# Optimization experiments

Hardware: AMD Instinct MI355X
Metric: run time of the kernel (lower is better)

The kernel has to match this reference:

```python
import jax, jax.numpy as jnp
import numpy as np
from jax import lax

B, C, L = 8, 512, 4096
G, K = 4, 3
PAD = 1
EPS = 1e-5


def setup_inputs() -> dict:
    key = jax.random.key(0)
    ks = jax.random.split(key, 8)
    inp = {
        "input_feat": jax.random.normal(ks[0], (B, C, L), dtype=jnp.float32),
        "x": jax.random.normal(ks[1], (B, C, L), dtype=jnp.float32),
        # depthwise Conv1d(channels, channels, k=3, pad=1, groups=channels): weight (C,1,K)
        "conv_w": jax.random.normal(ks[2], (C, 1, K), dtype=jnp.float32) * (1.0 / np.sqrt(K)),
        "conv_b": jax.random.normal(ks[3], (C,), dtype=jnp.float32) * 0.02,
        # BatchNorm1d affine params (module maps 'LN' -> BatchNorm1d)
        "bn_gamma": jnp.ones((C,), dtype=jnp.float32),
        "bn_beta": jnp.zeros((C,), dtype=jnp.float32),
        # offset/weight generators: Linear(C -> G*K). Source inits to zero (degenerate);
        # use small random values so the deformable path is exercised.
        "off_w": jax.random.normal(ks[4], (G * K, C), dtype=jnp.float32) * 0.02,
        "off_b": jax.random.normal(ks[5], (G * K,), dtype=jnp.float32) * 0.02,
        "wgt_w": jax.random.normal(ks[6], (G * K, C), dtype=jnp.float32) * 0.02,
        "wgt_b": jax.random.normal(ks[7], (G * K,), dtype=jnp.float32) * 0.02,
    }
    return inp


def _forward(x, conv_w, conv_b, bn_gamma, bn_beta, off_w, off_b, wgt_w, wgt_b):
    Bx, Cx, Lx = x.shape
    gs = Cx // G  # group size along channel axis

    # --- spectral_conv: depthwise conv1d + BatchNorm (batch stats) + exact GELU ---
    y = lax.conv_general_dilated(
        x, conv_w, window_strides=(1,), padding=[(PAD, PAD)],
        dimension_numbers=("NCH", "OIH", "NCH"), feature_group_count=Cx,
    ) + conv_b[None, :, None]
    mean = jnp.mean(y, axis=(0, 2), keepdims=True)
    var = jnp.var(y, axis=(0, 2), keepdims=True)
    y = (y - mean) * lax.rsqrt(var + EPS) * bn_gamma[None, :, None] + bn_beta[None, :, None]
    y = jax.nn.gelu(y, approximate=False)  # torch nn.GELU default is exact erf

    feat = y.transpose(0, 2, 1)  # (B, L, C)
    offsets = (feat @ off_w.T + off_b).reshape(Bx, Lx, G, K)
    weights = jax.nn.softmax((feat @ wgt_w.T + wgt_b).reshape(Bx, Lx, G, K), axis=-1)

    # --- deformable spectral gather + bilinear interp + softmax blend ---
    xg = x.transpose(0, 2, 1).reshape(Bx, Lx, G, gs)  # (B, L, G, gs)
    base = jnp.arange(gs, dtype=x.dtype)
    # sample positions: (B, L, G, K, gs)
    idx = jnp.clip(base[None, None, None, None, :] + offsets[..., None], 0.0, gs - 1)
    fl = jnp.floor(idx)
    frac = idx - fl
    fli = jnp.clip(fl, 0, gs - 1).astype(jnp.int32)
    cei = jnp.clip(jnp.ceil(idx), 0, gs - 1).astype(jnp.int32)

    xe = jnp.broadcast_to(xg[:, :, :, None, :], idx.shape)  # (B, L, G, K, gs)
    x_floor = jnp.take_along_axis(xe, fli, axis=-1)
    x_ceil = jnp.take_along_axis(xe, cei, axis=-1)
    interp = x_floor * (1.0 - frac) + x_ceil * frac  # (B, L, G, K, gs)

    out = jnp.sum(interp * weights[..., None], axis=3)  # (B, L, G, gs)
    return out.reshape(Bx, Lx, Cx).transpose(0, 2, 1)  # (B, C, L)


def reference(input_feat, x, conv_w, conv_b, bn_gamma, bn_beta, off_w, off_b, wgt_w, wgt_b):
    # input_feat is accepted but unused, matching the source forward signature.
    return _forward(x, conv_w, conv_b, bn_gamma, bn_beta, off_w, off_b, wgt_w, wgt_b)
```

## Files before the change

kernel.cpp:

```cpp
#include <hip/hip_runtime.h>
#include <math.h>

#define BB 8
#define CC 512
#define LL 4096
#define GG 4
#define KK 3
#define EPSV 1e-5f

#define TL 32
#define FTP 520
#define XGW 136

#define WB_F32OFF 9216

typedef float  f32x4_t  __attribute__((ext_vector_type(4)));
typedef __bf16 bf16x8_t __attribute__((ext_vector_type(8)));

__device__ __forceinline__ float gelu_tanh(float z) {
    float z2 = z * z;
    float a  = 1.5957691216f * fmaf(0.044715f * z2, z, z);
    return z * __builtin_amdgcn_rcpf(1.f + __expf(-a));
}

__device__ __forceinline__ ushort f32_to_bf16(float f) {
    uint u = __float_as_uint(f);
    return (ushort)((u + 0x7fffu + ((u >> 16) & 1u)) >> 16);
}

__device__ __forceinline__ float bf16_to_f32(ushort h) {
    return __uint_as_float((uint)h << 16);
}

__device__ __forceinline__ f32x4_t mfma_bf16(uint4 a, uint4 b, f32x4_t c) {
    return __builtin_amdgcn_mfma_f32_16x16x32_bf16(
        __builtin_bit_cast(bf16x8_t, a), __builtin_bit_cast(bf16x8_t, b), c, 0, 0, 0);
}

__global__ __launch_bounds__(256) void conv_stats_kernel(
    const float* __restrict__ x, const float* __restrict__ conv_w,
    const float* __restrict__ conv_b, float* __restrict__ ws)
{
    const int c = blockIdx.x;
    const int b = blockIdx.y;
    const int t = threadIdx.x;

    const float w0 = conv_w[c * 3 + 0];
    const float w1 = conv_w[c * 3 + 1];
    const float w2 = conv_w[c * 3 + 2];
    const float cb = conv_b[c];
    const float* xr = x + ((size_t)b * CC + c) * LL;

    float s = 0.f, ss = 0.f;
#pragma unroll
    for (int i = 0; i < 4; ++i) {
        const int l0 = 4 * (t + 256 * i);
        float4 q = *reinterpret_cast<const float4*>(xr + l0);
        float lf = __shfl_up(q.w, 1);
        if ((t & 63) == 0) lf = (l0 == 0) ? 0.f : xr[l0 - 1];
        float rt = __shfl_down(q.x, 1);
        if ((t & 63) == 63) rt = (l0 + 4 >= LL) ? 0.f : xr[l0 + 4];
        float y;
        y = fmaf(w0, lf,  fmaf(w1, q.x, fmaf(w2, q.y, cb))); s += y; ss = fmaf(y, y, ss);
        y = fmaf(w0, q.x, fmaf(w1, q.y, fmaf(w2, q.z, cb))); s += y; ss = fmaf(y, y, ss);
        y = fmaf(w0, q.y, fmaf(w1, q.z, fmaf(w2, q.w, cb))); s += y; ss = fmaf(y, y, ss);
        y = fmaf(w0, q.z, fmaf(w1, q.w, fmaf(w2, rt,  cb))); s += y; ss = fmaf(y, y, ss);
    }

#pragma unroll
    for (int d = 32; d > 0; d >>= 1) {
        s  += __shfl_down(s,  d, 64);
        ss += __shfl_down(ss, d, 64);
    }
    __shared__ float ls[4], lss[4];
    const int wid = t >> 6, lane = t & 63;
    if (lane == 0) { ls[wid] = s; lss[wid] = ss; }
    __syncthreads();
    if (t == 0) {
        ws[c * 8 + b]        = ls[0] + ls[1] + ls[2] + ls[3];
        ws[4096 + c * 8 + b] = lss[0] + lss[1] + lss[2] + lss[3];
    }
}

__global__ __launch_bounds__(512) void bn_finalize_kernel(
    const float* __restrict__ bn_gamma, const float* __restrict__ bn_beta,
    const float* __restrict__ off_w, const float* __restrict__ wgt_w,
    float* __restrict__ ws)
{
    const int t = threadIdx.x;
    {
        const int c = t;
        float s = 0.f, ss = 0.f;
#pragma unroll
        for (int b = 0; b < 8; ++b) {
            s  += ws[c * 8 + b];
            ss += ws[4096 + c * 8 + b];
        }
        const float inv  = 1.f / (float)(BB * LL);
        const float mean = s * inv;
        const float var  = ss * inv - mean * mean;
        const float sc   = bn_gamma[c] * rsqrtf(var + EPSV);
        ws[8192 + c] = sc;
        ws[8704 + c] = bn_beta[c] - mean * sc;
    }
    ushort* wb = reinterpret_cast<ushort*>(ws + WB_F32OFF);
    const int o  = t >> 4;
    const int k0 = (t & 15) * 32;
    uint* dst = reinterpret_cast<uint*>(wb + o * CC + k0);
    if (o < 24) {
        const float* src = (o < 12) ? (off_w + o * CC + k0) : (wgt_w + (o - 12) * CC + k0);
#pragma unroll 4
        for (int j = 0; j < 16; ++j) {
            float2 v = *reinterpret_cast<const float2*>(src + 2 * j);
            dst[j] = (uint)f32_to_bf16(v.x) | ((uint)f32_to_bf16(v.y) << 16);
        }
    } else {
#pragma unroll 4
        for (int j = 0; j < 16; ++j) dst[j] = 0u;
    }
}

__global__ __launch_bounds__(512, 4) void mega_kernel(
    const float* __restrict__ x,
    const float* __restrict__ conv_w, const float* __restrict__ conv_b,
    const float* __restrict__ off_b,  const float* __restrict__ wgt_b,
    const float* __restrict__ ws, float* __restrict__ out)
{
    __shared__ ushort xt[TL][GG][XGW];
    __shared__ ushort ftb[TL][FTP];
    __shared__ float  pr[TL][24];
    __shared__ float  W6[TL][GG][6];

    const int t  = threadIdx.x;
    const int b  = blockIdx.y;
    const int bx = blockIdx.x;
    const int ltile = ((bx & 7) << 4) | (bx >> 3);
    const int l0 = ltile * TL;

    {
        const int ch = t;
        const int g  = ch >> 7;
        const int j  = ch & 127;
        const float* xr = x + ((size_t)b * CC + ch) * LL + l0;
        const float w0 = conv_w[ch*3+0], w1 = conv_w[ch*3+1], w2 = conv_w[ch*3+2];
        const float sc = ws[8192 + ch];
        const float sh = fmaf(conv_b[ch], sc, ws[8704 + ch]);

        float cz = 0.f;
        float cw = (l0 == 0) ? 0.f : xr[-1];
#pragma unroll
        for (int i = 0; i < 8; ++i) {
            float4 q = *reinterpret_cast<const float4*>(xr + 4 * i);
            xt[4*i+0][g][3+j] = f32_to_bf16(q.x);
            xt[4*i+1][g][3+j] = f32_to_bf16(q.y);
            xt[4*i+2][g][3+j] = f32_to_bf16(q.z);
            xt[4*i+3][g][3+j] = f32_to_bf16(q.w);
            if (i > 0) {
                float cv = fmaf(w0, cz, fmaf(w1, cw, w2 * q.x));
                ftb[4*i-1][ch] = f32_to_bf16(gelu_tanh(fmaf(sc, cv, sh)));
            }
            float c0 = fmaf(w0, cw,  fmaf(w1, q.x, w2 * q.y));
            ftb[4*i+0][ch] = f32_to_bf16(gelu_tanh(fmaf(sc, c0, sh)));
            float c1 = fmaf(w0, q.x, fmaf(w1, q.y, w2 * q.z));
            ftb[4*i+1][ch] = f32_to_bf16(gelu_tanh(fmaf(sc, c1, sh)));
            float c2 = fmaf(w0, q.y, fmaf(w1, q.z, w2 * q.w));
            ftb[4*i+2][ch] = f32_to_bf16(gelu_tanh(fmaf(sc, c2, sh)));
            cz = q.z; cw = q.w;
        }
        float e2 = (l0 + TL >= LL) ? 0.f : xr[TL];
        float cv = fmaf(w0, cz, fmaf(w1, cw, w2 * e2));
        ftb[TL-1][ch] = f32_to_bf16(gelu_tanh(fmaf(sc, cv, sh)));

        if (j == 0) {
#pragma unroll
            for (int l = 0; l < TL; ++l) {
                ushort v = xt[l][g][3];
                xt[l][g][0] = v; xt[l][g][1] = v; xt[l][g][2] = v;
            }
        }
        if (j == 127) {
#pragma unroll
            for (int l = 0; l < TL; ++l) {
                ushort v = xt[l][g][130];
                xt[l][g][131] = v; xt[l][g][132] = v; xt[l][g][133] = v;
            }
        }
    }
    __syncthreads();

    const int wv = t >> 6, lane = t & 63;
    if (wv < 4) {
        const int msub = wv >> 1;
        const int n    = lane & 15;
        const int kb   = (lane >> 4) * 8;
        const ushort* wrow = reinterpret_cast<const ushort*>(ws + WB_F32OFF)
                             + ((wv & 1) * 16 + n) * CC + kb;
        const ushort* arow = &ftb[msub * 16 + n][kb];
        f32x4_t acc = {0.f, 0.f, 0.f, 0.f};
#pragma unroll
        for (int s = 0; s < CC / 32; ++s) {
            uint4 av = *reinterpret_cast<const uint4*>(arow + 32 * s);
            uint4 bv = *reinterpret_cast<const uint4*>(wrow + 32 * s);
            acc = mfma_bf16(av, bv, acc);
        }
        const int o = (wv & 1) * 16 + n;
        if (o < 24) {
            float bias = (o < 12) ? off_b[o] : wgt_b[o - 12];
            const int rb = (lane >> 4) * 4;
#pragma unroll
            for (int i = 0; i < 4; ++i) pr[msub * 16 + rb + i][o] = acc[i] + bias;
        }
    }
    __syncthreads();

    if (t < TL * GG) {
        const int l = t >> 2, g = t & 3;
        float s0 = pr[l][12 + g*3 + 0];
        float s1 = pr[l][12 + g*3 + 1];
        float s2 = pr[l][12 + g*3 + 2];
        float m  = fmaxf(s0, fmaxf(s1, s2));
        float e0 = __expf(s0 - m), e1 = __expf(s1 - m), e2 = __expf(s2 - m);
        float inv = __builtin_amdgcn_rcpf(e0 + e1 + e2);
        float wks[3] = {e0 * inv, e1 * inv, e2 * inv};
        float w6_0 = 0.f, w6_1 = 0.f, w6_2 = 0.f, w6_3 = 0.f, w6_4 = 0.f, w6_5 = 0.f;
#pragma unroll
        for (int k = 0; k < KK; ++k) {
            float off = pr[l][g*3 + k];
            float fo  = floorf(off);
            float fr  = off - fo;
            int d = (int)fo + 3;
            d = min(max(d, 0), 4);
            float wa = wks[k] * (1.f - fr);
            float wb = wks[k] * fr;
            w6_0 += (d == 0) ? wa : 0.f;
            w6_1 += (d == 1) ? wa : 0.f;  w6_1 += (d == 0) ? wb : 0.f;
            w6_2 += (d == 2) ? wa : 0.f;  w6_2 += (d == 1) ? wb : 0.f;
            w6_3 += (d == 3) ? wa : 0.f;  w6_3 += (d == 2) ? wb : 0.f;
            w6_4 += (d == 4) ? wa : 0.f;  w6_4 += (d == 3) ? wb : 0.f;
            w6_5 += (d == 4) ? wb : 0.f;
        }
        W6[l][g][0] = w6_0; W6[l][g][1] = w6_1; W6[l][g][2] = w6_2;
        W6[l][g][3] = w6_3; W6[l][g][4] = w6_4; W6[l][g][5] = w6_5;
    }
    __syncthreads();

    {
        const int ch = t, g = ch >> 7, j = ch & 127;
        float* orow = out + ((size_t)b * CC + ch) * LL + l0;
#pragma unroll
        for (int h = 0; h < 4; ++h) {
            float acc[8];
#pragma unroll
            for (int u = 0; u < 8; ++u) {
                const int l = h * 8 + u;
                const ushort* xr2 = &xt[l][g][j];
                const float*  w6  = &W6[l][g][0];
                float a = w6[0] * bf16_to_f32(xr2[0]);
                a = fmaf(w6[1], bf16_to_f32(xr2[1]), a);
                a = fmaf(w6[2], bf16_to_f32(xr2[2]), a);
                a = fmaf(w6[3], bf16_to_f32(xr2[3]), a);
                a = fmaf(w6[4], bf16_to_f32(xr2[4]), a);
                a = fmaf(w6[5], bf16_to_f32(xr2[5]), a);
                acc[u] = a;
            }
#pragma unroll
            for (int i = 0; i < 2; ++i) {
                *reinterpret_cast<float4*>(orow + h * 8 + 4 * i) =
                    make_float4(acc[4*i], acc[4*i+1], acc[4*i+2], acc[4*i+3]);
            }
        }
    }
}

extern "C" void kernel_launch(void* const* d_in, const int* in_sizes, int n_in,
                              void* d_out, int out_size, void* d_ws, size_t ws_size,
                              hipStream_t stream) {
    const float* x      = (const float*)d_in[1];
    const float* conv_w = (const float*)d_in[2];
    const float* conv_b = (const float*)d_in[3];
    const float* bn_g   = (const float*)d_in[4];
    const float* bn_b   = (const float*)d_in[5];
    const float* off_w  = (const float*)d_in[6];
    const float* off_b  = (const float*)d_in[7];
    const float* wgt_w  = (const float*)d_in[8];
    const float* wgt_b  = (const float*)d_in[9];
    float* out = (float*)d_out;
    float* ws  = (float*)d_ws;

    conv_stats_kernel<<<dim3(CC, BB), 256, 0, stream>>>(x, conv_w, conv_b, ws);
    bn_finalize_kernel<<<1, 512, 0, stream>>>(bn_g, bn_b, off_w, wgt_w, ws);
    mega_kernel<<<dim3(LL / TL, BB), 512, 0, stream>>>(
        x, conv_w, conv_b, off_b, wgt_b, ws, out);
}
```

Before: 223.4 us.

## Reuse one shared buffer for features and channel-major x with swizzled layout

The separate x-tile and feature tiles become one shared buffer, cutting LDS per block, and the launch-bounds occupancy hint rises from 4 to 8 blocks. The x tile is now stored channel-major, packed bf16 with an XOR swizzle, and reloaded from global after the GEMM phase instead of during the conv phase. The final blend is remapped so each thread writes float4 outputs for 4 positions using vectorized LDS reads, with W6 transposed for float4 access. The cost is a second global read of the x tile and more register pressure under the tighter launch bound.

```diff
diff --git a/kernel.cpp b/kernel.cpp
--- a/kernel.cpp
+++ b/kernel.cpp
@@ -10,7 +10,8 @@
 
 #define TL 32
 #define FTP 520
-#define XGW 136
+#define XROWS 134
+#define UNI_USHORTS (GG * XROWS * 32)
 
 #define WB_F32OFF 9216
 
@@ -28,8 +29,11 @@
     return (ushort)((u + 0x7fffu + ((u >> 16) & 1u)) >> 16);
 }
 
-__device__ __forceinline__ float bf16_to_f32(ushort h) {
-    return __uint_as_float((uint)h << 16);
+__device__ __forceinline__ float bf16_lo(uint u) { return __uint_as_float(u << 16); }
+__device__ __forceinline__ float bf16_hi(uint u) { return __uint_as_float(u & 0xffff0000u); }
+
+__device__ __forceinline__ uint pack2(float a, float b) {
+    return (uint)f32_to_bf16(a) | ((uint)f32_to_bf16(b) << 16);
 }
 
 __device__ __forceinline__ f32x4_t mfma_bf16(uint4 a, uint4 b, f32x4_t c) {
@@ -112,7 +116,7 @@
 #pragma unroll 4
         for (int j = 0; j < 16; ++j) {
             float2 v = *reinterpret_cast<const float2*>(src + 2 * j);
-            dst[j] = (uint)f32_to_bf16(v.x) | ((uint)f32_to_bf16(v.y) << 16);
+            dst[j] = pack2(v.x, v.y);
         }
     } else {
 #pragma unroll 4
@@ -120,16 +124,15 @@
     }
 }
 
-__global__ __launch_bounds__(512, 4) void mega_kernel(
+__global__ __launch_bounds__(512, 8) void mega_kernel(
     const float* __restrict__ x,
     const float* __restrict__ conv_w, const float* __restrict__ conv_b,
     const float* __restrict__ off_b,  const float* __restrict__ wgt_b,
     const float* __restrict__ ws, float* __restrict__ out)
 {
-    __shared__ ushort xt[TL][GG][XGW];
-    __shared__ ushort ftb[TL][FTP];
+    __shared__ ushort uni[UNI_USHORTS];
     __shared__ float  pr[TL][24];
-    __shared__ float  W6[TL][GG][6];
+    __shared__ float  W6[GG][6][TL];
 
     const int t  = threadIdx.x;
     const int b  = blockIdx.y;
@@ -137,11 +140,12 @@
     const int ltile = ((bx & 7) << 4) | (bx >> 3);
     const int l0 = ltile * TL;
 
+    const int ch = t;
+    const int g  = ch >> 7;
+    const int j  = ch & 127;
+    const float* xr = x + ((size_t)b * CC + ch) * LL + l0;
+
     {
-        const int ch = t;
-        const int g  = ch >> 7;
-        const int j  = ch & 127;
-        const float* xr = x + ((size_t)b * CC + ch) * LL + l0;
         const float w0 = conv_w[ch*3+0], w1 = conv_w[ch*3+1], w2 = conv_w[ch*3+2];
         const float sc = ws[8192 + ch];
         const float sh = fmaf(conv_b[ch], sc, ws[8704 + ch]);
@@ -151,40 +155,21 @@
 #pragma unroll
         for (int i = 0; i < 8; ++i) {
             float4 q = *reinterpret_cast<const float4*>(xr + 4 * i);
-            xt[4*i+0][g][3+j] = f32_to_bf16(q.x);
-            xt[4*i+1][g][3+j] = f32_to_bf16(q.y);
-            xt[4*i+2][g][3+j] = f32_to_bf16(q.z);
-            xt[4*i+3][g][3+j] = f32_to_bf16(q.w);
             if (i > 0) {
                 float cv = fmaf(w0, cz, fmaf(w1, cw, w2 * q.x));
-                ftb[4*i-1][ch] = f32_to_bf16(gelu_tanh(fmaf(sc, cv, sh)));
+                uni[(4*i-1) * FTP + ch] = f32_to_bf16(gelu_tanh(fmaf(sc, cv, sh)));
             }
             float c0 = fmaf(w0, cw,  fmaf(w1, q.x, w2 * q.y));
-            ftb[4*i+0][ch] = f32_to_bf16(gelu_tanh(fmaf(sc, c0, sh)));
+            uni[(4*i+0) * FTP + ch] = f32_to_bf16(gelu_tanh(fmaf(sc, c0, sh)));
             float c1 = fmaf(w0, q.x, fmaf(w1, q.y, w2 * q.z));
-            ftb[4*i+1][ch] = f32_to_bf16(gelu_tanh(fmaf(sc, c1, sh)));
+            uni[(4*i+1) * FTP + ch] = f32_to_bf16(gelu_tanh(fmaf(sc, c1, sh)));
             float c2 = fmaf(w0, q.y, fmaf(w1, q.z, w2 * q.w));
-            ftb[4*i+2][ch] = f32_to_bf16(gelu_tanh(fmaf(sc, c2, sh)));
+            uni[(4*i+2) * FTP + ch] = f32_to_bf16(gelu_tanh(fmaf(sc, c2, sh)));
             cz = q.z; cw = q.w;
         }
         float e2 = (l0 + TL >= LL) ? 0.f : xr[TL];
         float cv = fmaf(w0, cz, fmaf(w1, cw, w2 * e2));
-        ftb[TL-1][ch] = f32_to_bf16(gelu_tanh(fmaf(sc, cv, sh)));
-
-        if (j == 0) {
-#pragma unroll
-            for (int l = 0; l < TL; ++l) {
-                ushort v = xt[l][g][3];
-                xt[l][g][0] = v; xt[l][g][1] = v; xt[l][g][2] = v;
-            }
-        }
-        if (j == 127) {
-#pragma unroll
-            for (int l = 0; l < TL; ++l) {
-                ushort v = xt[l][g][130];
-                xt[l][g][131] = v; xt[l][g][132] = v; xt[l][g][133] = v;
-            }
-        }
+        uni[(TL-1) * FTP + ch] = f32_to_bf16(gelu_tanh(fmaf(sc, cv, sh)));
     }
     __syncthreads();
 
@@ -195,7 +180,7 @@
         const int kb   = (lane >> 4) * 8;
         const ushort* wrow = reinterpret_cast<const ushort*>(ws + WB_F32OFF)
                              + ((wv & 1) * 16 + n) * CC + kb;
-        const ushort* arow = &ftb[msub * 16 + n][kb];
+        const ushort* arow = &uni[(msub * 16 + n) * FTP + kb];
         f32x4_t acc = {0.f, 0.f, 0.f, 0.f};
 #pragma unroll
         for (int s = 0; s < CC / 32; ++s) {
@@ -213,61 +198,92 @@
     }
     __syncthreads();
 
+    {
+        const int rf  = g * XROWS + 3 + j;
+        const int key = rf & 3;
+        uint4* ubase = reinterpret_cast<uint4*>(uni);
+        uint4 chunks[4];
+#pragma unroll
+        for (int w = 0; w < 4; ++w) {
+            float4 qa = *reinterpret_cast<const float4*>(xr + 8 * w);
+            float4 qb = *reinterpret_cast<const float4*>(xr + 8 * w + 4);
+            chunks[w] = make_uint4(pack2(qa.x, qa.y), pack2(qa.z, qa.w),
+                                   pack2(qb.x, qb.y), pack2(qb.z, qb.w));
+            ubase[rf * 4 + (w ^ key)] = chunks[w];
+        }
+        if (j == 0) {
+#pragma unroll
+            for (int p = 0; p < 3; ++p) {
+                const int r2 = g * XROWS + p, k2 = r2 & 3;
+#pragma unroll
+                for (int w = 0; w < 4; ++w) ubase[r2 * 4 + (w ^ k2)] = chunks[w];
+            }
+        }
+        if (j == 127) {
+#pragma unroll
+            for (int p = 0; p < 3; ++p) {
+                const int r2 = g * XROWS + 131 + p, k2 = r2 & 3;
+#pragma unroll
+                for (int w = 0; w < 4; ++w) ubase[r2 * 4 + (w ^ k2)] = chunks[w];
+            }
+        }
+    }
     if (t < TL * GG) {
-        const int l = t >> 2, g = t & 3;
-        float s0 = pr[l][12 + g*3 + 0];
-        float s1 = pr[l][12 + g*3 + 1];
-        float s2 = pr[l][12 + g*3 + 2];
+        const int l = t >> 2, gg = t & 3;
+        float s0 = pr[l][12 + gg*3 + 0];
+        float s1 = pr[l][12 + gg*3 + 1];
+        float s2 = pr[l][12 + gg*3 + 2];
         float m  = fmaxf(s0, fmaxf(s1, s2));
         float e0 = __expf(s0 - m), e1 = __expf(s1 - m), e2 = __expf(s2 - m);
         float inv = __builtin_amdgcn_rcpf(e0 + e1 + e2);
         float wks[3] = {e0 * inv, e1 * inv, e2 * inv};
-        float w6_0 = 0.f, w6_1 = 0.f, w6_2 = 0.f, w6_3 = 0.f, w6_4 = 0.f, w6_5 = 0.f;
+        float w6v[6] = {0.f, 0.f, 0.f, 0.f, 0.f, 0.f};
 #pragma unroll
         for (int k = 0; k < KK; ++k) {
-            float off = pr[l][g*3 + k];
+            float off = pr[l][gg*3 + k];
             float fo  = floorf(off);
             float fr  = off - fo;
             int d = (int)fo + 3;
             d = min(max(d, 0), 4);
             float wa = wks[k] * (1.f - fr);
             float wb = wks[k] * fr;
-            w6_0 += (d == 0) ? wa : 0.f;
-            w6_1 += (d == 1) ? wa : 0.f;  w6_1 += (d == 0) ? wb : 0.f;
-            w6_2 += (d == 2) ? wa : 0.f;  w6_2 += (d == 1) ? wb : 0.f;
-            w6_3 += (d == 3) ? wa : 0.f;  w6_3 += (d == 2) ? wb : 0.f;
-            w6_4 += (d == 4) ? wa : 0.f;  w6_4 += (d == 3) ? wb : 0.f;
-            w6_5 += (d == 4) ? wb : 0.f;
-        }
-        W6[l][g][0] = w6_0; W6[l][g][1] = w6_1; W6[l][g][2] = w6_2;
-        W6[l][g][3] = w6_3; W6[l][g][4] = w6_4; W6[l][g][5] = w6_5;
+#pragma unroll
+            for (int q = 0; q < 5; ++q) w6v[q] += (d == q) ? wa : 0.f;
+#pragma unroll
+            for (int q = 1; q < 6; ++q) w6v[q] += (d == q - 1) ? wb : 0.f;
+        }
+#pragma unroll
+        for (int q = 0; q < 6; ++q) W6[gg][q][l] = w6v[q];
     }
     __syncthreads();
 
     {
-        const int ch = t, g = ch >> 7, j = ch & 127;
-        float* orow = out + ((size_t)b * CC + ch) * LL + l0;
-#pragma unroll
-        for (int h = 0; h < 4; ++h) {
-            float acc[8];
-#pragma unroll
-            for (int u = 0; u < 8; ++u) {
-                const int l = h * 8 + u;
-                const ushort* xr2 = &xt[l][g][j];
-                const float*  w6  = &W6[l][g][0];
-                float a = w6[0] * bf16_to_f32(xr2[0]);
-                a = fmaf(w6[1], bf16_to_f32(xr2[1]), a);
-                a = fmaf(w6[2], bf16_to_f32(xr2[2]), a);
-                a = fmaf(w6[3], bf16_to_f32(xr2[3]), a);
-                a = fmaf(w6[4], bf16_to_f32(xr2[4]), a);
-                a = fmaf(w6[5], bf16_to_f32(xr2[5]), a);
-                acc[u] = a;
-            }
-#pragma unroll
-            for (int i = 0; i < 2; ++i) {
-                *reinterpret_cast<float4*>(orow + h * 8 + 4 * i) =
-                    make_float4(acc[4*i], acc[4*i+1], acc[4*i+2], acc[4*i+3]);
-            }
+        const int rbase = t >> 3;
+        const int l     = (t & 7) * 4;
+        float4 w6c[6];
+#pragma unroll
+        for (int i = 0; i < 8; ++i) {
+            const int r  = rbase + 64 * i;
+            const int gi = r >> 7;
+            const int ji = r & 127;
+            if ((i & 1) == 0) {
+#pragma unroll
+                for (int d = 0; d < 6; ++d)
+                    w6c[d] = *reinterpret_cast<const float4*>(&W6[gi][d][l]);
+            }
+            float ax = 0.f, ay = 0.f, az = 0.f, aw = 0.f;
+#pragma unroll
+            for (int d = 0; d < 6; ++d) {
+                const int rf2 = gi * XROWS + ji + d;
+                const int idx = rf2 * 32 + (l ^ ((rf2 & 3) << 3));
+                uint2 u = *reinterpret_cast<const uint2*>(&uni[idx]);
+                ax = fmaf(w6c[d].x, bf16_lo(u.x), ax);
+                ay = fmaf(w6c[d].y, bf16_hi(u.x), ay);
+                az = fmaf(w6c[d].z, bf16_lo(u.y), az);
+                aw = fmaf(w6c[d].w, bf16_hi(u.y), aw);
+            }
+            *reinterpret_cast<float4*>(out + ((size_t)b * CC + r) * LL + l0 + l) =
+                make_float4(ax, ay, az, aw);
         }
     }
 }
```

Result: faster. 203.6 us (-8.9%).
